# Kernel optimization log

Hardware: AMD Instinct MI355X
Metric: run time of the kernel (lower is better)

## Reference

```python
import jax, jax.numpy as jnp
import numpy as np
import math

K = 20        # args.k  (global-branch neighbors)
KL = 20       # args.kl (local-branch neighbors)
EPS = 1e-5    # BatchNorm eps
SLOPE = 0.2   # LeakyReLU slope


def _knn(x, k, keep):
    # x: [B,C,N]; keep: [B,N] bool column mask. pd = -||xi - xj||^2.
    xx = jnp.sum(x * x, axis=1)                          # [B,N]
    inner = jnp.einsum('bci,bcj->bij', x, x)             # [B,N,N]
    pd = 2.0 * inner - xx[:, :, None] - xx[:, None, :]
    mn = jnp.min(pd, axis=-1)                            # per-row min
    # suppressed columns are set to the row min so topk never selects them
    pd = jnp.where(keep[:, None, :], pd, mn[:, :, None])
    return jax.lax.top_k(pd, k)[1]                       # [B,N,k]


def _gather(pts, idx):
    # pts: [B,N,C], idx: [B,N,k] -> [B,N,k,C]
    b = jnp.arange(pts.shape[0])[:, None, None]
    return pts[b, idx]


def _edge_feat(x, k, keep, smooth):
    # DGCNN edge features: concat(neighbor - center, center) -> [B,2C,N,k]
    idx = _knn(x, k, keep)
    xp = jnp.transpose(x, (0, 2, 1))                     # [B,N,C]
    if smooth:
        # GraphLayer: neighbors come from a topk-mean smoothed field
        knn_x = _gather(xp, idx)                         # [B,N,k,C]
        k2 = math.ceil(k * 2 / 3)
        top = jax.lax.top_k(jnp.transpose(knn_x, (0, 1, 3, 2)), k2)[0]
        src = jnp.mean(top, axis=-1)                     # [B,N,C]
    else:
        src = xp
    feat = _gather(src, idx)                             # [B,N,k,C]
    ctr = jnp.broadcast_to(xp[:, :, None, :], feat.shape)
    out = jnp.concatenate([feat - ctr, ctr], axis=-1)    # [B,N,k,2C]
    return jnp.transpose(out, (0, 3, 1, 2))


def _bn(y, axes):
    # BatchNorm (training-mode batch stats, gamma=1, beta=0 as at init)
    mu = jnp.mean(y, axis=axes, keepdims=True)
    var = jnp.var(y, axis=axes, keepdims=True)
    return (y - mu) * jax.lax.rsqrt(var + EPS)


def _conv_block(x, w, axes):
    # 1x1 conv (no bias) + BN + LeakyReLU
    ein = 'oc,bcnk->bonk' if x.ndim == 4 else 'oc,bcn->bon'
    return jax.nn.leaky_relu(_bn(jnp.einsum(ein, w, x), axes), SLOPE)


def _forward(x, local_idx, w1, w2, w3, w4, w5, w6, w7, w8, w9,
             l1w, l2w, l2b, l3w, l3b):
    keep_l = local_idx
    keep_g = jnp.logical_not(local_idx)
    ax4 = (0, 2, 3)
    # local (smoothed GraphLayer) branch, neighbors restricted to local points
    xl1 = _conv_block(_edge_feat(x,   KL, keep_l, True), w1, ax4).max(-1)
    xl2 = _conv_block(_edge_feat(xl1, KL, keep_l, True), w2, ax4).max(-1)
    xl3 = _conv_block(_edge_feat(xl2, KL, keep_l, True), w3, ax4).max(-1)
    xl4 = _conv_block(_edge_feat(xl3, KL, keep_l, True), w4, ax4).max(-1)
    x_local = jnp.concatenate([xl1, xl2, xl3, xl4], axis=1)  # [B,512,N]
    # global branch, neighbors restricted to non-local points
    xg1 = _conv_block(_edge_feat(x,   K, keep_g, False), w5, ax4).max(-1)
    xg2 = _conv_block(_edge_feat(xg1, K, keep_g, False), w6, ax4).max(-1)
    xg3 = _conv_block(_edge_feat(xg2, K, keep_g, False), w7, ax4).max(-1)
    xg4 = _conv_block(_edge_feat(xg3, K, keep_g, False), w8, ax4).max(-1)
    x_glob = jnp.concatenate([xg1, xg2, xg3, xg4], axis=1)   # [B,512,N]
    # per-point merge: local columns take the local-branch features
    h = jnp.where(local_idx[:, None, :], x_local, x_glob)
    h = _conv_block(h, w9, (0, 2))                            # [B,E,N]
    g = jnp.concatenate([h.max(-1), h.mean(-1)], axis=1)      # [B,2E]
    # head: linears + BN1d + LeakyReLU; dropout is identity (eval mode)
    g = jax.nn.leaky_relu(_bn(g @ l1w.T, (0,)), SLOPE)
    g = jax.nn.leaky_relu(_bn(g @ l2w.T + l2b, (0,)), SLOPE)
    return g @ l3w.T + l3b


def setup_inputs() -> dict:
    key = jax.random.key(0)
    ks = jax.random.split(key, 16)
    B, N, E, OUT = 4, 2048, 1024, 40

    def w(k, o, i):
        return jax.random.normal(k, (o, i), jnp.float32) / np.sqrt(i)

    return {
        'x': jax.random.normal(ks[0], (B, 3, N), jnp.float32),
        'local_idx': jax.random.bernoulli(ks[1], 0.5, (B, N)),
        'geod_dist': jax.random.normal(ks[2], (B, N), jnp.float32),
        'w1': w(ks[3], 64, 6),   'w2': w(ks[4], 64, 128),
        'w3': w(ks[5], 128, 128), 'w4': w(ks[6], 256, 256),
        'w5': w(ks[7], 64, 6),   'w6': w(ks[8], 64, 128),
        'w7': w(ks[9], 128, 128), 'w8': w(ks[10], 256, 256),
        'w9': w(ks[11], E, 512),
        'l1w': w(ks[12], 512, 2 * E),
        'l2w': w(ks[13], 256, 512),
        'l2b': jnp.zeros((256,), jnp.float32),
        'l3w': w(ks[14], OUT, 256),
        'l3b': jnp.zeros((OUT,), jnp.float32),
    }


def reference(x, local_idx, geod_dist, w1, w2, w3, w4, w5, w6, w7, w8, w9,
              l1w, l2w, l2b, l3w, l3b):
    del geod_dist  # accepted but unused in the original forward
    return _forward(x, local_idx, w1, w2, w3, w4, w5, w6, w7, w8, w9,
                    l1w, l2w, l2b, l3w, l3b)
```

## Files before the change

### kernel.cpp

```cpp
#include <hip/hip_runtime.h>
#include <hip/hip_bf16.h>
#include <cfloat>

#define BB 4
#define NN 2048
#define KNN 20
#define KTOP 14
#define EPSBN 1e-5f
#define SLOPE 0.2f

__global__ void k_xx3(const float* __restrict__ x, float* __restrict__ xx) {
  int t = blockIdx.x * 64 + threadIdx.x;
  int b = t >> 11, n = t & 2047;
  const float* xb = x + (long)b * (3L * NN) + n;
  float v0 = xb[0], v1 = xb[NN], v2 = xb[2 * NN];
  xx[t] = v0 * v0 + v1 * v1 + v2 * v2;
}

__device__ __forceinline__ void suppress(float* __restrict__ trow,
                                         const int* __restrict__ lrow,
                                         int keepv, int lane) {
  int base = 4 * lane;
#pragma unroll
  for (int q = 0; q < 8; ++q) {
    float4 lv = *(const float4*)(trow + 256 * q + base);
    int4 kv = *(const int4*)(lrow + 256 * q + base);
    lv.x = (((kv.x != 0) ? 1 : 0) == keepv) ? lv.x : -FLT_MAX;
    lv.y = (((kv.y != 0) ? 1 : 0) == keepv) ? lv.y : -FLT_MAX;
    lv.z = (((kv.z != 0) ? 1 : 0) == keepv) ? lv.z : -FLT_MAX;
    lv.w = (((kv.w != 0) ? 1 : 0) == keepv) ? lv.w : -FLT_MAX;
    *(float4*)(trow + 256 * q + base) = lv;
  }
}

__device__ __forceinline__ void sel_lds(float* __restrict__ trow, int lane,
                                        int* __restrict__ orow) {
  int base = 4 * lane;
  for (int t = 0; t < KNN; ++t) {
    float v[32];
#pragma unroll
    for (int q = 0; q < 8; ++q) {
      float4 lv = *(const float4*)(trow + 256 * q + base);
      v[4 * q + 0] = lv.x; v[4 * q + 1] = lv.y;
      v[4 * q + 2] = lv.z; v[4 * q + 3] = lv.w;
    }
    float mv[16]; int mi[16];
#pragma unroll
    for (int s = 0; s < 16; ++s) {
      mi[s] = (v[2 * s] >= v[2 * s + 1]) ? 2 * s : 2 * s + 1;
      mv[s] = fmaxf(v[2 * s], v[2 * s + 1]);
    }
#pragma unroll
    for (int s = 0; s < 8; ++s) {
      mi[s] = (mv[2 * s] >= mv[2 * s + 1]) ? mi[2 * s] : mi[2 * s + 1];
      mv[s] = fmaxf(mv[2 * s], mv[2 * s + 1]);
    }
#pragma unroll
    for (int s = 0; s < 4; ++s) {
      mi[s] = (mv[2 * s] >= mv[2 * s + 1]) ? mi[2 * s] : mi[2 * s + 1];
      mv[s] = fmaxf(mv[2 * s], mv[2 * s + 1]);
    }
    int i01 = (mv[0] >= mv[1]) ? mi[0] : mi[1];
    float v01 = fmaxf(mv[0], mv[1]);
    int i23 = (mv[2] >= mv[3]) ? mi[2] : mi[3];
    float v23 = fmaxf(mv[2], mv[3]);
    int li = (v01 >= v23) ? i01 : i23;
    float bv = fmaxf(v01, v23);
    float gv = bv;
#pragma unroll
    for (int d = 1; d < 64; d <<= 1) gv = fmaxf(gv, __shfl_xor(gv, d));
    unsigned long long mk = __ballot(bv == gv);
    int wl = (int)(__ffsll((long long)mk) - 1);
    int jloc = 256 * (li >> 2) + base + (li & 3);
    int bj = __shfl(jloc, wl);
    if (lane == 0) { orow[t] = bj; trow[bj] = -FLT_MAX; }
  }
}

template <int C>
__device__ __forceinline__ void knn_body(
    float (*tile)[NN], float (*a_lds)[4],
    const float* __restrict__ xb, const float* __restrict__ xxb,
    const int* __restrict__ lrow, int i0, int keepv,
    int* __restrict__ orowbase, int tid, int wid, int lane) {
  for (int jt = 0; jt < NN; jt += 1024) {
    float acc[4][4];
#pragma unroll
    for (int r = 0; r < 4; ++r)
#pragma unroll
      for (int s = 0; s < 4; ++s) acc[r][s] = 0.f;
#pragma unroll 4
    for (int c = 0; c < C; ++c) {
      float4 a = *(const float4*)&a_lds[c][0];
      float4 h = *(const float4*)&xb[(long)c * NN + jt + tid * 4];
      acc[0][0] += a.x * h.x; acc[0][1] += a.x * h.y; acc[0][2] += a.x * h.z; acc[0][3] += a.x * h.w;
      acc[1][0] += a.y * h.x; acc[1][1] += a.y * h.y; acc[1][2] += a.y * h.z; acc[1][3] += a.y * h.w;
      acc[2][0] += a.z * h.x; acc[2][1] += a.z * h.y; acc[2][2] += a.z * h.z; acc[2][3] += a.z * h.w;
      acc[3][0] += a.w * h.x; acc[3][1] += a.w * h.y; acc[3][2] += a.w * h.z; acc[3][3] += a.w * h.w;
    }
    float4 xxj = *(const float4*)&xxb[jt + tid * 4];
#pragma unroll
    for (int r = 0; r < 4; ++r) {
      float xxi = xxb[i0 + r];
      float4 o;
      o.x = 2.f * acc[r][0] - xxi - xxj.x;
      o.y = 2.f * acc[r][1] - xxi - xxj.y;
      o.z = 2.f * acc[r][2] - xxi - xxj.z;
      o.w = 2.f * acc[r][3] - xxi - xxj.w;
      *(float4*)&tile[r][jt + tid * 4] = o;
    }
  }
  __syncthreads();
  float* trow = &tile[wid][0];
  suppress(trow, lrow, keepv, lane);
  sel_lds(trow, lane, orowbase);
}

template <int C>
__global__ __launch_bounds__(256) void k_knn_dual(
    const float* __restrict__ xbase, long bstride, const float* __restrict__ xxbase,
    const int* __restrict__ lidx,
    int* __restrict__ idxA , int* __restrict__ idxB ) {
  __shared__ float tile[4][NN];
  __shared__ float a_lds[C][4];
  int b = blockIdx.y;
  int i0 = blockIdx.x * 4;
  const float* xb = xbase + (long)b * bstride;
  const float* xxb = xxbase + b * NN;
  int tid = threadIdx.x, wid = tid >> 6, lane = tid & 63;
  for (int t = tid; t < 4 * C; t += 256) {
    int c = t >> 2, r = t & 3;
    a_lds[c][r] = xb[(long)c * NN + i0 + r];
  }
  __syncthreads();
  const int* lrow = lidx + b * NN;
  int i = i0 + wid;
  knn_body<C>(tile, a_lds, xb, xxb, lrow, i0, 1,
              idxA + ((long)b * NN + i) * KNN, tid, wid, lane);
  __syncthreads();
  knn_body<C>(tile, a_lds, xb, xxb, lrow, i0, 0,
              idxB + ((long)b * NN + i) * KNN, tid, wid, lane);
}

template <int C>
__global__ __launch_bounds__(256) void k_knn2(
    const float* __restrict__ xA, const float* __restrict__ xxA,
    int* __restrict__ idxA,
    const float* __restrict__ xB, const float* __restrict__ xxB,
    int* __restrict__ idxB, long bstride, const int* __restrict__ lidx) {
  __shared__ float tile[4][NN];
  __shared__ float a_lds[C][4];
  int half = blockIdx.z;
  const float* xbase = half ? xB : xA;
  const float* xxbase = half ? xxB : xxA;
  int keepv = half ? 0 : 1;
  int* idxO = half ? idxB : idxA;
  int b = blockIdx.y;
  int i0 = blockIdx.x * 4;
  const float* xb = xbase + (long)b * bstride;
  const float* xxb = xxbase + b * NN;
  int tid = threadIdx.x, wid = tid >> 6, lane = tid & 63;
  for (int t = tid; t < 4 * C; t += 256) {
    int c = t >> 2, r = t & 3;
    a_lds[c][r] = xb[(long)c * NN + i0 + r];
  }
  __syncthreads();
  const int* lrow = lidx + b * NN;
  int i = i0 + wid;
  knn_body<C>(tile, a_lds, xb, xxb, lrow, i0, keepv,
              idxO + ((long)b * NN + i) * KNN, tid, wid, lane);
}

__global__ void k_smooth(const float* __restrict__ x, long bstride, int C,
                         const int* __restrict__ idx, float* __restrict__ src) {
  long t = (long)blockIdx.x * blockDim.x + threadIdx.x;
  if (t >= (long)BB * C * NN) return;
  int n = (int)(t % NN);
  int c = (int)((t / NN) % C);
  int b = (int)(t / ((long)NN * C));
  const int* id = idx + ((long)b * NN + n) * KNN;
  const float* xb = x + (long)b * bstride + (long)c * NN;
  float v[KNN]; float sum = 0.f;
#pragma unroll
  for (int kk = 0; kk < KNN; ++kk) { v[kk] = xb[id[kk]]; sum += v[kk]; }
  int r0 = -1, r1 = -1, r2 = -1, r3 = -1, r4 = -1, r5 = -1;
#pragma unroll
  for (int r = 0; r < KNN - KTOP; ++r) {
    float mvv = FLT_MAX; int mi = -1;
#pragma unroll
    for (int j = 0; j < KNN; ++j) {
      if (j == r0 || j == r1 || j == r2 || j == r3 || j == r4 || j == r5) continue;
      if (v[j] < mvv) { mvv = v[j]; mi = j; }
    }
    sum -= mvv;
    if (r == 0) r0 = mi; else if (r == 1) r1 = mi; else if (r == 2) r2 = mi;
    else if (r == 3) r3 = mi; else if (r == 4) r4 = mi; else r5 = mi;
  }
  src[((long)b * C + c) * NN + n] = sum * (1.f / KTOP);
}

__global__ void k_wprep_all(
    const float* __restrict__ w1, const float* __restrict__ w2,
    const float* __restrict__ w3, const float* __restrict__ w4,
    const float* __restrict__ w5, const float* __restrict__ w6,
    const float* __restrict__ w7, const float* __restrict__ w8,
    float* __restrict__ wa, float* __restrict__ wd) {
  int L = blockIdx.y;
  const float* w; int O, C; long off;
  switch (L) {
    case 0: w = w1; O = 64;  C = 3;   off = 0;     break;
    case 1: w = w2; O = 64;  C = 64;  off = 192;   break;
    case 2: w = w3; O = 128; C = 64;  off = 4288;  break;
    case 3: w = w4; O = 256; C = 128; off = 12480; break;
    case 4: w = w5; O = 64;  C = 3;   off = 45248; break;
    case 5: w = w6; O = 64;  C = 64;  off = 45440; break;
    case 6: w = w7; O = 128; C = 64;  off = 49536; break;
    default: w = w8; O = 256; C = 128; off = 57728; break;
  }
  for (int t = blockIdx.x * blockDim.x + threadIdx.x; t < O * C;
       t += gridDim.x * blockDim.x) {
    int o = t / C, c = t % C;
    float a = w[(long)o * 2 * C + c];
    float bb = w[(long)o * 2 * C + C + c];
    wa[off + (long)c * O + o] = a;
    wd[off + (long)c * O + o] = bb - a;
  }
}

template <int C>
__global__ __launch_bounds__(256) void k_zt2(
    const float* __restrict__ Ma, long mas,
    const float* __restrict__ Mb_, long mbs,
    const float* __restrict__ wa, const float* __restrict__ wd,
    int O, float* __restrict__ Zs, float* __restrict__ Zd) {
  constexpr int KC = (C >= 16) ? 16 : C;
  __shared__ float As[KC][64], Bs[KC][64];
  int z = blockIdx.z;
  int nyo = gridDim.y >> 1;
  int half = (blockIdx.y >= nyo) ? 1 : 0;
  int o0 = (half ? (blockIdx.y - nyo) : blockIdx.y) * 64;
  const float* M = half ? Mb_ : Ma;
  long ms = half ? mbs : mas;
  const float* Wt = half ? wd : wa;
  float* T = half ? Zd : Zs;
  const float* Mb = M + (long)z * ms;
  float* Tb = T + (long)z * NN * O;
  int tid = threadIdx.x;
  int tx = tid & 15, ty = tid >> 4;
  int n0 = blockIdx.x * 64;
  float acc[4][4];
#pragma unroll
  for (int r = 0; r < 4; ++r)
#pragma unroll
    for (int s = 0; s < 4; ++s) acc[r][s] = 0.f;
  for (int c0 = 0; c0 < C; c0 += KC) {
    for (int e = tid; e < KC * 64; e += 256) {
      int c = e >> 6, ii = e & 63;
      As[c][ii] = Mb[(long)(c0 + c) * NN + n0 + ii];
      Bs[c][ii] = Wt[(long)(c0 + c) * O + o0 + ii];
    }
    __syncthreads();
#pragma unroll
    for (int cc = 0; cc < KC; ++cc) {
      float4 a = *(const float4*)&As[cc][ty * 4];
      float4 h = *(const float4*)&Bs[cc][tx * 4];
      acc[0][0] += a.x * h.x; acc[0][1] += a.x * h.y; acc[0][2] += a.x * h.z; acc[0][3] += a.x * h.w;
      acc[1][0] += a.y * h.x; acc[1][1] += a.y * h.y; acc[1][2] += a.y * h.z; acc[1][3] += a.y * h.w;
      acc[2][0] += a.z * h.x; acc[2][1] += a.z * h.y; acc[2][2] += a.z * h.z; acc[2][3] += a.z * h.w;
      acc[3][0] += a.w * h.x; acc[3][1] += a.w * h.y; acc[3][2] += a.w * h.z; acc[3][3] += a.w * h.w;
    }
    __syncthreads();
  }
#pragma unroll
  for (int r = 0; r < 4; ++r) {
    float4 v; v.x = acc[r][0]; v.y = acc[r][1]; v.z = acc[r][2]; v.w = acc[r][3];
    *(float4*)&Tb[(long)(n0 + ty * 4 + r) * O + o0 + tx * 4] = v;
  }
}

template <int O, int PTS>
__global__ __launch_bounds__(O) void k_gmax(
    const float* __restrict__ Zs, const float* __restrict__ Zd,
    const int* __restrict__ idx, float* __restrict__ ymax,
    float* __restrict__ stats) {
  int tid = threadIdx.x;
  int bn0 = blockIdx.x * PTS;
  int b = bn0 >> 11;
  long zbase = (long)b * NN * O;
  float ss = 0.f, sq = 0.f;
  for (int p = 0; p < PTS; ++p) {
    int bn = bn0 + p;
    const int* ir = idx + (long)bn * KNN;
    float zd = Zd[(long)bn * O + tid];
    float smax = -FLT_MAX;
#pragma unroll
    for (int k = 0; k < KNN; ++k) {
      float y = Zs[zbase + (long)ir[k] * O + tid] + zd;
      smax = fmaxf(smax, y); ss += y; sq += y * y;
    }
    ymax[(long)bn * O + tid] = smax;
  }
  atomicAdd(&stats[tid], ss);
  atomicAdd(&stats[O + tid], sq);
}

__global__ void k_bnmax(const float* __restrict__ ymax, const float* __restrict__ stats,
                        int O, float invcnt, float* __restrict__ out, long out_bstride,
                        float* __restrict__ xxout) {
  long t = (long)blockIdx.x * blockDim.x + threadIdx.x;
  if (t >= (long)BB * O * NN) return;
  int n = (int)(t % NN);
  int o = (int)((t / NN) % O);
  int b = (int)(t / ((long)NN * O));
  float mu = stats[o] * invcnt;
  float var = stats[O + o] * invcnt - mu * mu;
  float rs = rsqrtf(var + EPSBN);
  float v = (ymax[((long)b * NN + n) * O + o] - mu) * rs;
  v = v >= 0.f ? v : SLOPE * v;
  out[(long)b * out_bstride + (long)o * NN + n] = v;
  if (xxout) atomicAdd(&xxout[b * NN + n], v * v);
}

__global__ __launch_bounds__(256) void k_gemm9(
    const float* __restrict__ W, const float* __restrict__ xl,
    const float* __restrict__ xg, const int* __restrict__ lidx,
    float* __restrict__ h2, float* __restrict__ stats) {
  __shared__ float Ws[16][72];
  __shared__ float Hs[16][132];
  int tid = threadIdx.x;
  int tx = tid & 31, ty = tid >> 5;
  int p0 = blockIdx.x * 128, o0 = blockIdx.y * 64;
  int b = p0 >> 11, n0 = p0 & 2047;
  int sp = tid & 127, scq = (tid >> 7) * 8;
  const float* hbase;
  {
    int pt = p0 + sp;
    hbase = (lidx[pt] ? xl : xg) + (long)b * (512L * NN) + (pt & 2047);
  }
  int wo = tid >> 2, wc = (tid & 3) * 4;
  float acc[8][4];
#pragma unroll
  for (int i = 0; i < 8; ++i)
#pragma unroll
    for (int j = 0; j < 4; ++j) acc[i][j] = 0.f;

  for (int c0 = 0; c0 < 512; c0 += 16) {
    float4 wv = *(const float4*)(W + (long)(o0 + wo) * 512 + c0 + wc);
    Ws[wc + 0][wo] = wv.x; Ws[wc + 1][wo] = wv.y;
    Ws[wc + 2][wo] = wv.z; Ws[wc + 3][wo] = wv.w;
    long crow = (long)(c0 + scq) * NN;
#pragma unroll
    for (int e = 0; e < 8; ++e) Hs[scq + e][sp] = hbase[crow + (long)e * NN];
    __syncthreads();
#pragma unroll
    for (int cc = 0; cc < 16; ++cc) {
      float4 a0 = *(const float4*)&Ws[cc][ty * 8];
      float4 a1 = *(const float4*)&Ws[cc][ty * 8 + 4];
      float4 h = *(const float4*)&Hs[cc][tx * 4];
      acc[0][0] += a0.x * h.x; acc[0][1] += a0.x * h.y; acc[0][2] += a0.x * h.z; acc[0][3] += a0.x * h.w;
      acc[1][0] += a0.y * h.x; acc[1][1] += a0.y * h.y; acc[1][2] += a0.y * h.z; acc[1][3] += a0.y * h.w;
      acc[2][0] += a0.z * h.x; acc[2][1] += a0.z * h.y; acc[2][2] += a0.z * h.z; acc[2][3] += a0.z * h.w;
      acc[3][0] += a0.w * h.x; acc[3][1] += a0.w * h.y; acc[3][2] += a0.w * h.z; acc[3][3] += a0.w * h.w;
      acc[4][0] += a1.x * h.x; acc[4][1] += a1.x * h.y; acc[4][2] += a1.x * h.z; acc[4][3] += a1.x * h.w;
      acc[5][0] += a1.y * h.x; acc[5][1] += a1.y * h.y; acc[5][2] += a1.y * h.z; acc[5][3] += a1.y * h.w;
      acc[6][0] += a1.z * h.x; acc[6][1] += a1.z * h.y; acc[6][2] += a1.z * h.z; acc[6][3] += a1.z * h.w;
      acc[7][0] += a1.w * h.x; acc[7][1] += a1.w * h.y; acc[7][2] += a1.w * h.z; acc[7][3] += a1.w * h.w;
    }
    __syncthreads();
  }
#pragma unroll
  for (int i = 0; i < 8; ++i) {
    int o = o0 + ty * 8 + i;
    float4 v; v.x = acc[i][0]; v.y = acc[i][1]; v.z = acc[i][2]; v.w = acc[i][3];
    *(float4*)&h2[((long)b * 1024 + o) * NN + n0 + tx * 4] = v;
    float ss = acc[i][0] + acc[i][1] + acc[i][2] + acc[i][3];
    float sq = acc[i][0] * acc[i][0] + acc[i][1] * acc[i][1] +
               acc[i][2] * acc[i][2] + acc[i][3] * acc[i][3];
    for (int d = 16; d > 0; d >>= 1) {
      ss += __shfl_down(ss, d, 32);
      sq += __shfl_down(sq, d, 32);
    }
    if (tx == 0) {
      atomicAdd(&stats[o], ss);
      atomicAdd(&stats[1024 + o], sq);
    }
  }
}

__global__ void k_gpool(const float* __restrict__ h2, const float* __restrict__ stats,
                        float* __restrict__ g) {
  int b = blockIdx.x / 1024, o = blockIdx.x % 1024;
  int tid = threadIdx.x;
  float mu = stats[o] * (1.f / 8192.f);
  float var = stats[1024 + o] * (1.f / 8192.f) - mu * mu;
  float rs = rsqrtf(var + EPSBN);
  const float* hr = h2 + ((long)b * 1024 + o) * NN;
  float mx = -FLT_MAX, sm = 0.f;
  for (int n = tid; n < NN; n += 256) {
    float v = (hr[n] - mu) * rs; v = v >= 0.f ? v : SLOPE * v;
    mx = fmaxf(mx, v); sm += v;
  }
  __shared__ float smx[256], ssm[256];
  smx[tid] = mx; ssm[tid] = sm; __syncthreads();
  for (int s = 128; s > 0; s >>= 1) {
    if (tid < s) { smx[tid] = fmaxf(smx[tid], smx[tid + s]); ssm[tid] += ssm[tid + s]; }
    __syncthreads();
  }
  if (tid == 0) { g[b * 2048 + o] = smx[0]; g[b * 2048 + 1024 + o] = ssm[0] * (1.f / NN); }
}

__global__ void k_head(const float* __restrict__ gin, int CIN, const float* __restrict__ wl,
                       const float* __restrict__ bias, float* __restrict__ gout, int do_bn) {
  int f = blockIdx.x, tid = threadIdx.x, F = gridDim.x;
  const float* wr = wl + (long)f * CIN;
  float a0 = 0, a1 = 0, a2 = 0, a3 = 0;
  for (int c = tid; c < CIN; c += 256) {
    float wv = wr[c];
    a0 += wv * gin[c];         a1 += wv * gin[CIN + c];
    a2 += wv * gin[2 * CIN + c]; a3 += wv * gin[3 * CIN + c];
  }
  __shared__ float s0[256], s1[256], s2[256], s3[256];
  s0[tid] = a0; s1[tid] = a1; s2[tid] = a2; s3[tid] = a3; __syncthreads();
  for (int s = 128; s > 0; s >>= 1) {
    if (tid < s) { s0[tid] += s0[tid + s]; s1[tid] += s1[tid + s];
                   s2[tid] += s2[tid + s]; s3[tid] += s3[tid + s]; }
    __syncthreads();
  }
  if (tid == 0) {
    float z0 = s0[0], z1 = s1[0], z2 = s2[0], z3 = s3[0];
    if (bias) { float bb = bias[f]; z0 += bb; z1 += bb; z2 += bb; z3 += bb; }
    if (do_bn) {
      float mu = 0.25f * (z0 + z1 + z2 + z3);
      float var = 0.25f * (z0 * z0 + z1 * z1 + z2 * z2 + z3 * z3) - mu * mu;
      float rs = rsqrtf(var + EPSBN);
      z0 = (z0 - mu) * rs; z1 = (z1 - mu) * rs; z2 = (z2 - mu) * rs; z3 = (z3 - mu) * rs;
      z0 = z0 >= 0.f ? z0 : SLOPE * z0; z1 = z1 >= 0.f ? z1 : SLOPE * z1;
      z2 = z2 >= 0.f ? z2 : SLOPE * z2; z3 = z3 >= 0.f ? z3 : SLOPE * z3;
    }
    gout[0 * F + f] = z0; gout[1 * F + f] = z1; gout[2 * F + f] = z2; gout[3 * F + f] = z3;
  }
}

extern "C" void kernel_launch(void* const* d_in, const int* in_sizes, int n_in,
                              void* d_out, int out_size, void* d_ws, size_t ws_size,
                              hipStream_t stream) {
  const float* x   = (const float*)d_in[0];
  const int*   lidx= (const int*)d_in[1];
  const float* w1  = (const float*)d_in[3];
  const float* w2  = (const float*)d_in[4];
  const float* w3  = (const float*)d_in[5];
  const float* w4  = (const float*)d_in[6];
  const float* w5  = (const float*)d_in[7];
  const float* w6  = (const float*)d_in[8];
  const float* w7  = (const float*)d_in[9];
  const float* w8  = (const float*)d_in[10];
  const float* w9  = (const float*)d_in[11];
  const float* l1w = (const float*)d_in[12];
  const float* l2w = (const float*)d_in[13];
  const float* l2b = (const float*)d_in[14];
  const float* l3w = (const float*)d_in[15];
  const float* l3b = (const float*)d_in[16];
  float* out = (float*)d_out;

  float* ws    = (float*)d_ws;
  float* xxall = ws;
  float* stats = ws + 57344;
  int*   idxb  = (int*)(ws + 61440);
  float* xloc  = ws + 225280;
  float* xglb  = ws + 4419584;
  float* big   = ws + 8613888;
  float* g     = ws + 17002496;
  float* g1    = ws + 17010688;
  float* g2    = ws + 17012736;
  float* waall = ws + 17013760;
  float* wdall = ws + 17104256;

  float* srcb  = big;
  float* Zs    = big + 1048576;
  float* Zd    = big + 3145728;
  float* ymaxb = big + 5242880;
  int*   idxG2 = (int*)(big + 7340032);
  float* h2    = big;
  int*   idxG  = (int*)xglb;

  float* xxS0 = xxall;
  float* xxS1 = xxall + 8192;
  float* xxS2 = xxall + 16384;
  float* xxS3 = xxall + 24576;
  float* xxS4 = xxall + 32768;
  float* xxS5 = xxall + 40960;
  float* xxS6 = xxall + 49152;

  float* SL1 = stats + 0;    float* SL2 = stats + 128;
  float* SL3 = stats + 256;  float* SL4 = stats + 512;
  float* SG1 = stats + 1024; float* SG2 = stats + 1152;
  float* SG3 = stats + 1280; float* SG4 = stats + 1536;
  float* S9  = stats + 2048;

  const float invE = 1.f / (BB * NN * KNN);
  const long XS0 = 3L * NN;
  const long XS  = 512L * NN;
  const dim3 gknn(NN / 4, BB);
  const dim3 gknn2(NN / 4, BB, 2);

  hipMemsetAsync(ws, 0, 61440 * sizeof(float), stream);
  k_wprep_all<<<dim3(128, 8), 256, 0, stream>>>(w1, w2, w3, w4, w5, w6, w7, w8,
                                                waall, wdall);
  k_xx3<<<128, 64, 0, stream>>>(x, xxS0);

  k_knn_dual<3><<<gknn, 256, 0, stream>>>(x, XS0, xxS0, lidx, idxb, idxG);

  k_smooth<<<(BB * 3 * NN + 255) / 256, 256, 0, stream>>>(x, XS0, 3, idxb, srcb);
  k_zt2<3><<<dim3(32, 2, 4), 256, 0, stream>>>(srcb, 3L * NN, x, XS0,
                                               waall + 0, wdall + 0, 64, Zs, Zd);
  k_gmax<64, 8><<<BB * NN / 8, 64, 0, stream>>>(Zs, Zd, idxb, ymaxb, SL1);
  k_bnmax<<<(BB * 64 * NN + 255) / 256, 256, 0, stream>>>(ymaxb, SL1, 64, invE,
                                                          xloc + 0 * NN, XS, xxS1);
  k_zt2<3><<<dim3(32, 2, 4), 256, 0, stream>>>(x, XS0, x, XS0,
                                               waall + 45248, wdall + 45248, 64, Zs, Zd);
  k_gmax<64, 8><<<BB * NN / 8, 64, 0, stream>>>(Zs, Zd, idxG, ymaxb, SG1);
  k_bnmax<<<(BB * 64 * NN + 255) / 256, 256, 0, stream>>>(ymaxb, SG1, 64, invE,
                                                          xglb + 0 * NN, XS, xxS4);

  k_knn2<64><<<gknn2, 256, 0, stream>>>(xloc, xxS1, idxb,
                                        xglb, xxS4, idxG2, XS, lidx);
  k_smooth<<<(BB * 64 * NN + 255) / 256, 256, 0, stream>>>(xloc, XS, 64, idxb, srcb);
  k_zt2<64><<<dim3(32, 2, 4), 256, 0, stream>>>(srcb, 64L * NN, xloc, XS,
                                                waall + 192, wdall + 192, 64, Zs, Zd);
  k_gmax<64, 8><<<BB * NN / 8, 64, 0, stream>>>(Zs, Zd, idxb, ymaxb, SL2);
  k_bnmax<<<(BB * 64 * NN + 255) / 256, 256, 0, stream>>>(ymaxb, SL2, 64, invE,
                                                          xloc + 64 * NN, XS, xxS2);
  k_zt2<64><<<dim3(32, 2, 4), 256, 0, stream>>>(xglb, XS, xglb, XS,
                                                waall + 45440, wdall + 45440, 64, Zs, Zd);
  k_gmax<64, 8><<<BB * NN / 8, 64, 0, stream>>>(Zs, Zd, idxG2, ymaxb, SG2);
  k_bnmax<<<(BB * 64 * NN + 255) / 256, 256, 0, stream>>>(ymaxb, SG2, 64, invE,
                                                          xglb + 64 * NN, XS, xxS5);

  k_knn2<64><<<gknn2, 256, 0, stream>>>(xloc + 64 * NN, xxS2, idxb,
                                        xglb + 64 * NN, xxS5, idxG2, XS, lidx);
  k_smooth<<<(BB * 64 * NN + 255) / 256, 256, 0, stream>>>(xloc + 64 * NN, XS, 64, idxb, srcb);
  k_zt2<64><<<dim3(32, 4, 4), 256, 0, stream>>>(srcb, 64L * NN, xloc + 64 * NN, XS,
                                                waall + 4288, wdall + 4288, 128, Zs, Zd);
  k_gmax<128, 16><<<BB * NN / 16, 128, 0, stream>>>(Zs, Zd, idxb, ymaxb, SL3);
  k_bnmax<<<(BB * 128 * NN + 255) / 256, 256, 0, stream>>>(ymaxb, SL3, 128, invE,
                                                           xloc + 128 * NN, XS, xxS3);
  k_zt2<64><<<dim3(32, 4, 4), 256, 0, stream>>>(xglb + 64 * NN, XS, xglb + 64 * NN, XS,
                                                waall + 49536, wdall + 49536, 128, Zs, Zd);
  k_gmax<128, 16><<<BB * NN / 16, 128, 0, stream>>>(Zs, Zd, idxG2, ymaxb, SG3);
  k_bnmax<<<(BB * 128 * NN + 255) / 256, 256, 0, stream>>>(ymaxb, SG3, 128, invE,
                                                           xglb + 128 * NN, XS, xxS6);

  k_knn2<128><<<gknn2, 256, 0, stream>>>(xloc + 128 * NN, xxS3, idxb,
                                         xglb + 128 * NN, xxS6, idxG2, XS, lidx);
  k_smooth<<<(BB * 128 * NN + 255) / 256, 256, 0, stream>>>(xloc + 128 * NN, XS, 128, idxb, srcb);
  k_zt2<128><<<dim3(32, 8, 4), 256, 0, stream>>>(srcb, 128L * NN, xloc + 128 * NN, XS,
                                                 waall + 12480, wdall + 12480, 256, Zs, Zd);
  k_gmax<256, 16><<<BB * NN / 16, 256, 0, stream>>>(Zs, Zd, idxb, ymaxb, SL4);
  k_bnmax<<<(BB * 256 * NN + 255) / 256, 256, 0, stream>>>(ymaxb, SL4, 256, invE,
                                                           xloc + 256 * NN, XS, nullptr);
  k_zt2<128><<<dim3(32, 8, 4), 256, 0, stream>>>(xglb + 128 * NN, XS, xglb + 128 * NN, XS,
                                                 waall + 57728, wdall + 57728, 256, Zs, Zd);
  k_gmax<256, 16><<<BB * NN / 16, 256, 0, stream>>>(Zs, Zd, idxG2, ymaxb, SG4);
  k_bnmax<<<(BB * 256 * NN + 255) / 256, 256, 0, stream>>>(ymaxb, SG4, 256, invE,
                                                           xglb + 256 * NN, XS, nullptr);

  {
    dim3 g9(NN * BB / 128, 1024 / 64);
    k_gemm9<<<g9, 256, 0, stream>>>(w9, xloc, xglb, lidx, h2, S9);
  }
  k_gpool<<<BB * 1024, 256, 0, stream>>>(h2, S9, g);
  k_head<<<512, 256, 0, stream>>>(g, 2048, l1w, nullptr, g1, 1);
  k_head<<<256, 256, 0, stream>>>(g1, 512, l2w, l2b, g2, 1);
  k_head<<<40, 256, 0, stream>>>(g2, 256, l3w, l3b, out, 0);
}
```

Measured before the change: 1.219 ms.

## Keep kNN selection in registers with per-lane top-2 cache and compute distances once

Top-k selection no longer rescans the LDS row on every one of the 20 iterations. Each lane now holds its 32 candidates in registers and caches its top-2. Only the winning lane recomputes its local max, and only after both cached entries are used. The dual kernel also computes the pairwise-distance tile once and reuses it for both the local and global masks, where it was previously computed twice. The cost is more register pressure, and the refill step runs with divergent control flow.

```diff
diff --git a/kernel.cpp b/kernel.cpp
--- a/kernel.cpp
+++ b/kernel.cpp
@@ -17,72 +17,79 @@
   xx[t] = v0 * v0 + v1 * v1 + v2 * v2;
 }
 
-__device__ __forceinline__ void suppress(float* __restrict__ trow,
-                                         const int* __restrict__ lrow,
-                                         int keepv, int lane) {
+__device__ __forceinline__ void top1_tree(const float v[32], float& bv, int& bi) {
+  float mv[16]; int mi[16];
+#pragma unroll
+  for (int s = 0; s < 16; ++s) {
+    mi[s] = (v[2 * s] >= v[2 * s + 1]) ? 2 * s : 2 * s + 1;
+    mv[s] = fmaxf(v[2 * s], v[2 * s + 1]);
+  }
+#pragma unroll
+  for (int s = 0; s < 8; ++s) {
+    mi[s] = (mv[2 * s] >= mv[2 * s + 1]) ? mi[2 * s] : mi[2 * s + 1];
+    mv[s] = fmaxf(mv[2 * s], mv[2 * s + 1]);
+  }
+#pragma unroll
+  for (int s = 0; s < 4; ++s) {
+    mi[s] = (mv[2 * s] >= mv[2 * s + 1]) ? mi[2 * s] : mi[2 * s + 1];
+    mv[s] = fmaxf(mv[2 * s], mv[2 * s + 1]);
+  }
+  int i01 = (mv[0] >= mv[1]) ? mi[0] : mi[1];
+  float v01 = fmaxf(mv[0], mv[1]);
+  int i23 = (mv[2] >= mv[3]) ? mi[2] : mi[3];
+  float v23 = fmaxf(mv[2], mv[3]);
+  bi = (v01 >= v23) ? i01 : i23;
+  bv = fmaxf(v01, v23);
+}
+
+__device__ __forceinline__ void remove_slot(float v[32], int bi) {
+#pragma unroll
+  for (int s = 0; s < 32; ++s)
+    if (s == bi) v[s] = -FLT_MAX;
+}
+
+__device__ __forceinline__ void sel_reg(const float* __restrict__ trow,
+                                        const int* __restrict__ lrow,
+                                        int keepv, int lane,
+                                        int* __restrict__ orow) {
   int base = 4 * lane;
+  float v[32];
 #pragma unroll
   for (int q = 0; q < 8; ++q) {
     float4 lv = *(const float4*)(trow + 256 * q + base);
     int4 kv = *(const int4*)(lrow + 256 * q + base);
-    lv.x = (((kv.x != 0) ? 1 : 0) == keepv) ? lv.x : -FLT_MAX;
-    lv.y = (((kv.y != 0) ? 1 : 0) == keepv) ? lv.y : -FLT_MAX;
-    lv.z = (((kv.z != 0) ? 1 : 0) == keepv) ? lv.z : -FLT_MAX;
-    lv.w = (((kv.w != 0) ? 1 : 0) == keepv) ? lv.w : -FLT_MAX;
-    *(float4*)(trow + 256 * q + base) = lv;
-  }
-}
-
-__device__ __forceinline__ void sel_lds(float* __restrict__ trow, int lane,
-                                        int* __restrict__ orow) {
-  int base = 4 * lane;
+    v[4 * q + 0] = (((kv.x != 0) ? 1 : 0) == keepv) ? lv.x : -FLT_MAX;
+    v[4 * q + 1] = (((kv.y != 0) ? 1 : 0) == keepv) ? lv.y : -FLT_MAX;
+    v[4 * q + 2] = (((kv.z != 0) ? 1 : 0) == keepv) ? lv.z : -FLT_MAX;
+    v[4 * q + 3] = (((kv.w != 0) ? 1 : 0) == keepv) ? lv.w : -FLT_MAX;
+  }
+  float bv1, bv2; int li1, li2;
+  top1_tree(v, bv1, li1); remove_slot(v, li1);
+  top1_tree(v, bv2, li2); remove_slot(v, li2);
+  bool has2 = true;
   for (int t = 0; t < KNN; ++t) {
-    float v[32];
-#pragma unroll
-    for (int q = 0; q < 8; ++q) {
-      float4 lv = *(const float4*)(trow + 256 * q + base);
-      v[4 * q + 0] = lv.x; v[4 * q + 1] = lv.y;
-      v[4 * q + 2] = lv.z; v[4 * q + 3] = lv.w;
-    }
-    float mv[16]; int mi[16];
-#pragma unroll
-    for (int s = 0; s < 16; ++s) {
-      mi[s] = (v[2 * s] >= v[2 * s + 1]) ? 2 * s : 2 * s + 1;
-      mv[s] = fmaxf(v[2 * s], v[2 * s + 1]);
-    }
-#pragma unroll
-    for (int s = 0; s < 8; ++s) {
-      mi[s] = (mv[2 * s] >= mv[2 * s + 1]) ? mi[2 * s] : mi[2 * s + 1];
-      mv[s] = fmaxf(mv[2 * s], mv[2 * s + 1]);
-    }
-#pragma unroll
-    for (int s = 0; s < 4; ++s) {
-      mi[s] = (mv[2 * s] >= mv[2 * s + 1]) ? mi[2 * s] : mi[2 * s + 1];
-      mv[s] = fmaxf(mv[2 * s], mv[2 * s + 1]);
-    }
-    int i01 = (mv[0] >= mv[1]) ? mi[0] : mi[1];
-    float v01 = fmaxf(mv[0], mv[1]);
-    int i23 = (mv[2] >= mv[3]) ? mi[2] : mi[3];
-    float v23 = fmaxf(mv[2], mv[3]);
-    int li = (v01 >= v23) ? i01 : i23;
-    float bv = fmaxf(v01, v23);
-    float gv = bv;
+    float gv = bv1;
 #pragma unroll
     for (int d = 1; d < 64; d <<= 1) gv = fmaxf(gv, __shfl_xor(gv, d));
-    unsigned long long mk = __ballot(bv == gv);
+    unsigned long long mk = __ballot(bv1 == gv);
     int wl = (int)(__ffsll((long long)mk) - 1);
-    int jloc = 256 * (li >> 2) + base + (li & 3);
+    int jloc = 256 * (li1 >> 2) + base + (li1 & 3);
     int bj = __shfl(jloc, wl);
-    if (lane == 0) { orow[t] = bj; trow[bj] = -FLT_MAX; }
+    if (lane == 0) orow[t] = bj;
+    bool iwin = (lane == wl);
+    bool refill = iwin && !has2;
+    if (iwin && has2) { bv1 = bv2; li1 = li2; has2 = false; }
+    if (__ballot(refill)) {
+      if (refill) { top1_tree(v, bv1, li1); remove_slot(v, li1); }
+    }
   }
 }
 
 template <int C>
-__device__ __forceinline__ void knn_body(
+__device__ __forceinline__ void pd_tile(
     float (*tile)[NN], float (*a_lds)[4],
     const float* __restrict__ xb, const float* __restrict__ xxb,
-    const int* __restrict__ lrow, int i0, int keepv,
-    int* __restrict__ orowbase, int tid, int wid, int lane) {
+    int i0, int tid) {
   for (int jt = 0; jt < NN; jt += 1024) {
     float acc[4][4];
 #pragma unroll
@@ -110,10 +117,6 @@
       *(float4*)&tile[r][jt + tid * 4] = o;
     }
   }
-  __syncthreads();
-  float* trow = &tile[wid][0];
-  suppress(trow, lrow, keepv, lane);
-  sel_lds(trow, lane, orowbase);
 }
 
 template <int C>
@@ -133,13 +136,13 @@
     a_lds[c][r] = xb[(long)c * NN + i0 + r];
   }
   __syncthreads();
+  pd_tile<C>(tile, a_lds, xb, xxb, i0, tid);
+  __syncthreads();
   const int* lrow = lidx + b * NN;
   int i = i0 + wid;
-  knn_body<C>(tile, a_lds, xb, xxb, lrow, i0, 1,
-              idxA + ((long)b * NN + i) * KNN, tid, wid, lane);
-  __syncthreads();
-  knn_body<C>(tile, a_lds, xb, xxb, lrow, i0, 0,
-              idxB + ((long)b * NN + i) * KNN, tid, wid, lane);
+  const float* trow = &tile[wid][0];
+  sel_reg(trow, lrow, 1, lane, idxA + ((long)b * NN + i) * KNN);
+  sel_reg(trow, lrow, 0, lane, idxB + ((long)b * NN + i) * KNN);
 }
 
 template <int C>
@@ -165,10 +168,11 @@
     a_lds[c][r] = xb[(long)c * NN + i0 + r];
   }
   __syncthreads();
+  pd_tile<C>(tile, a_lds, xb, xxb, i0, tid);
+  __syncthreads();
   const int* lrow = lidx + b * NN;
   int i = i0 + wid;
-  knn_body<C>(tile, a_lds, xb, xxb, lrow, i0, keepv,
-              idxO + ((long)b * NN + i) * KNN, tid, wid, lane);
+  sel_reg(&tile[wid][0], lrow, keepv, lane, idxO + ((long)b * NN + i) * KNN);
 }
 
 __global__ void k_smooth(const float* __restrict__ x, long bstride, int C,
```

Result: slower. 1.391 ms (+14.1%).
